# Kernel tuning notes

Measured on AMD Instinct MI355X. Metric: run time of the kernel, lower is better.

The kernel has to match this reference:

```python
import jax, jax.numpy as jnp
import numpy as np

MAX_CH = 21
LAT_DIM = 64
D_EMBED = 1024
N_HEADS = 16
D_HEAD = D_EMBED // N_HEADS  # 64
L = MAX_CH * LAT_DIM         # 1344 latents
B, T = 4, 1024


def setup_inputs() -> dict:
    key = jax.random.key(0)
    k1, k2, k3, k4, k5, k6 = jax.random.split(key, 6)
    x = jax.random.normal(k1, (B, T, D_EMBED), dtype=jnp.float32)
    # boolean channel mask [b, L, T]
    ch_mask = jax.random.randint(k2, (B, L, T), 0, 2) > 0
    # learned latent queries [L, H*d] (xavier-uniform-ish init)
    lim_q = float(np.sqrt(6.0 / (L + N_HEADS * D_HEAD)))
    latent_q = jax.random.uniform(k3, (L, N_HEADS * D_HEAD), minval=-lim_q, maxval=lim_q, dtype=jnp.float32)
    # Linear weights (torch layout: [out, in]) and biases
    lim_w = float(np.sqrt(1.0 / D_EMBED))
    w_k_w = jax.random.uniform(k4, (N_HEADS * D_HEAD, D_EMBED), minval=-lim_w, maxval=lim_w, dtype=jnp.float32)
    w_k_b = jnp.zeros((N_HEADS * D_HEAD,), dtype=jnp.float32)
    w_v_w = jax.random.uniform(k5, (N_HEADS * D_HEAD, D_EMBED), minval=-lim_w, maxval=lim_w, dtype=jnp.float32)
    w_v_b = jax.random.uniform(k6, (N_HEADS * D_HEAD,), minval=-lim_w, maxval=lim_w, dtype=jnp.float32)
    return {"x": x, "ch_mask": ch_mask, "latent_q": latent_q,
            "w_k_w": w_k_w, "w_k_b": w_k_b, "w_v_w": w_v_w, "w_v_b": w_v_b}


def reference(x, ch_mask, latent_q, w_k_w, w_k_b, w_v_w, w_v_b):
    b, t, d = x.shape
    H, dh = N_HEADS, D_HEAD
    l = latent_q.shape[0]
    # faithful to torch .view(-1, H, L, d): raw row-major reinterpretation
    lq = latent_q.reshape(1, H, l, dh)                    # [1,H,L,dh]
    k = (x @ w_k_w.T + w_k_b).reshape(b, t, H, dh).transpose(0, 2, 3, 1)  # [b,H,dh,T]
    v = (x @ w_v_w.T + w_v_b).reshape(b, t, H, dh).transpose(0, 2, 1, 3)  # [b,H,T,dh]
    scale = jnp.float32(H) ** -0.5  # note: n_heads**-0.5, as in source
    scores = jnp.einsum('ohld,bhdt->bhlt', lq, k) * scale  # [b,H,L,T]
    mask = ch_mask[:, None, :, :]                           # [b,1,L,T] broadcast over heads
    scores = jnp.where(mask, scores, jnp.float32(-1e9))
    w = jax.nn.softmax(scores, axis=-1)
    w = jnp.where(mask, w, jnp.float32(0.0))
    out = jnp.einsum('bhlt,bhtd->bhld', w, v)               # [b,H,L,dh]
    return out.transpose(0, 2, 1, 3).reshape(b, l, H * dh)  # [b,L,H*dh]
```

## Files before the change

kernel.cpp:

```cpp
#include <hip/hip_runtime.h>
#include <hip/hip_bf16.h>

#define B_SZ 4
#define T_SZ 1024
#define NH 16
#define L_SZ 1344
#define LT_COUNT 21

typedef __attribute__((ext_vector_type(8))) short short8;
typedef __attribute__((ext_vector_type(4))) short short4v;
typedef __attribute__((ext_vector_type(4))) float floatx4;

typedef __attribute__((address_space(1))) const void gvoid;
typedef __attribute__((address_space(3))) void svoid;
#define GLD16(gp, lp) \
  __builtin_amdgcn_global_load_lds((gvoid*)(gp), (svoid*)(lp), 16, 0, 0)

static __device__ inline short bf16bits(float f) {
  return __builtin_bit_cast(short, __float2bfloat16(f));
}
static __device__ inline short4v cvt4(float4 v) {
  short4v r;
  r.x = bf16bits(v.x); r.y = bf16bits(v.y);
  r.z = bf16bits(v.z); r.w = bf16bits(v.w);
  return r;
}

static __device__ inline unsigned pack_bf16_2(float a, float b) {
  unsigned ua = __builtin_bit_cast(unsigned, a) + 0x8000u;
  unsigned ub = __builtin_bit_cast(unsigned, b) + 0x8000u;
  return __builtin_amdgcn_perm(ub, ua, 0x07060302u);
}
static __device__ inline uint2 pack_bf16_4(float4 v) {
  return make_uint2(pack_bf16_2(v.x, v.y), pack_bf16_2(v.z, v.w));
}


__global__ __launch_bounds__(256) void mask_detect(
    const unsigned char* __restrict__ m, int* __restrict__ flag) {
  __shared__ int any_off4, any_at4;
  if (threadIdx.x == 0) { any_off4 = 0; any_at4 = 0; }
  __syncthreads();
  int a1 = 0, a2 = 0;
  for (int i = threadIdx.x; i < 4096; i += 256) {
    unsigned char v = m[i];
    if (v) {
      if ((i & 3) != 0) a1 = 1;
      if ((i & 7) == 4) a2 = 1;
    }
  }
  if (a1) atomicOr(&any_off4, 1);
  if (a2) atomicOr(&any_at4, 1);
  __syncthreads();
  if (threadIdx.x == 0) *flag = any_off4 ? 1 : (any_at4 ? 0 : 2);
}

__global__ __launch_bounds__(256) void prep_kernel(
    const float4* __restrict__ x, const float4* __restrict__ wk,
    const float4* __restrict__ wv,
    uint2* __restrict__ xb, uint2* __restrict__ wkb, uint2* __restrict__ wvb,
    const void* __restrict__ mask, const int* __restrict__ flag,
    unsigned int* __restrict__ bits) {
  const int f = *flag;
  const int lane = threadIdx.x & 63;
  for (int vb = blockIdx.x; vb < 27648; vb += gridDim.x) {
    if (vb < 6144) {
      size_t i = (size_t)vb * 256 + threadIdx.x;
      if (i < 1048576)      xb[i] = pack_bf16_4(x[i]);
      else if (i < 1310720) wkb[i - 1048576] = pack_bf16_4(wk[i - 1048576]);
      else                  wvb[i - 1310720] = pack_bf16_4(wv[i - 1310720]);
    } else {
      int idx = (vb - 6144) * 256 + threadIdx.x;
      bool v;
      if (f == 1)      v = ((const signed char*)mask)[idx] != 0;
      else if (f == 2) v = ((const long long*)mask)[idx] != 0;
      else             v = ((const int*)mask)[idx] != 0;
      unsigned long long bal = __ballot(v);
      if ((lane & 31) == 0) {
        unsigned int w = (lane & 32) ? (unsigned int)(bal >> 32) : (unsigned int)bal;
        bits[idx >> 5] = w;
      }
    }
  }
}

__global__ __launch_bounds__(256, 4) void gemm_kv_bf16(
    const __hip_bfloat16* __restrict__ xb,
    const __hip_bfloat16* __restrict__ wkb, const __hip_bfloat16* __restrict__ wvb,
    const float* __restrict__ bk, const float* __restrict__ bv,
    __hip_bfloat16* __restrict__ k_buf, __hip_bfloat16* __restrict__ v_buf) {
  __shared__ __align__(16) __hip_bfloat16 ldsA[2][128 * 32];
  __shared__ __align__(16) __hip_bfloat16 ldsB[2][64 * 32];
  const int tid = threadIdx.x;
  const int lane = tid & 63, w = tid >> 6;
  const int wm = w & 1, wn = w >> 1;
  const int c15 = lane & 15, kq = lane >> 4;

  const __hip_bfloat16* A;
  const __hip_bfloat16* B;
  int TA, TB;
  if (blockIdx.z == 0) {
    A = wkb; B = xb; TA = blockIdx.x >> 6; TB = blockIdx.x & 63;
  } else {
    A = xb; B = wvb; TA = blockIdx.x >> 4; TB = blockIdx.x & 15;
  }
  const __hip_bfloat16* Abase = A + (size_t)TA * 128 * 1024;
  const __hip_bfloat16* Bbase = B + (size_t)TB * 64 * 1024;

  floatx4 acc[4][2];
  #pragma unroll
  for (int i = 0; i < 4; ++i)
    #pragma unroll
    for (int j = 0; j < 2; ++j) acc[i][j] = (floatx4){0.f, 0.f, 0.f, 0.f};

#define GSTAGE(sb, kk) do {                                                  \
    int cA_ = w * 128 + lane;                                                \
    int rA_ = cA_ >> 2, gA_ = (cA_ & 3) ^ (rA_ & 3);                         \
    GLD16(Abase + (size_t)rA_ * 1024 + (kk) + gA_ * 8,                       \
          &ldsA[sb][(w * 128) * 8]);                                         \
    int cA2_ = cA_ + 64;                                                     \
    int rA2_ = cA2_ >> 2, gA2_ = (cA2_ & 3) ^ (rA2_ & 3);                    \
    GLD16(Abase + (size_t)rA2_ * 1024 + (kk) + gA2_ * 8,                     \
          &ldsA[sb][(w * 128 + 64) * 8]);                                    \
    int cB_ = w * 64 + lane;                                                 \
    int rB_ = cB_ >> 2, gB_ = (cB_ & 3) ^ (rB_ & 3);                         \
    GLD16(Bbase + (size_t)rB_ * 1024 + (kk) + gB_ * 8,                       \
          &ldsB[sb][(w * 64) * 8]);                                          \
  } while (0)

  GSTAGE(0, 0);
  for (int kk = 0; kk < 1024; kk += 32) {
    const int buf = (kk >> 5) & 1;
    if (kk + 32 < 1024) {
      GSTAGE(buf ^ 1, kk + 32);
      asm volatile("s_waitcnt vmcnt(3)" ::: "memory");
    } else {
      asm volatile("s_waitcnt vmcnt(0)" ::: "memory");
    }
    __builtin_amdgcn_s_barrier();

    short8 af[4], bfr[2];
    #pragma unroll
    for (int mi = 0; mi < 4; ++mi) {
      int row = wm * 64 + mi * 16 + c15;
      af[mi] = *(const short8*)(&ldsA[buf][row * 32 + ((kq ^ (row & 3)) * 8)]);
    }
    #pragma unroll
    for (int ni = 0; ni < 2; ++ni) {
      int row = wn * 32 + ni * 16 + c15;
      bfr[ni] = *(const short8*)(&ldsB[buf][row * 32 + ((kq ^ (row & 3)) * 8)]);
    }
    #pragma unroll
    for (int mi = 0; mi < 4; ++mi)
      #pragma unroll
      for (int ni = 0; ni < 2; ++ni)
        acc[mi][ni] = __builtin_amdgcn_mfma_f32_16x16x32_bf16(
            af[mi], bfr[ni], acc[mi][ni], 0, 0, 0);

    asm volatile("s_waitcnt lgkmcnt(0)" ::: "memory");
    __builtin_amdgcn_s_barrier();
  }
#undef GSTAGE

  if (blockIdx.z == 0) {
    #pragma unroll
    for (int ni = 0; ni < 2; ++ni) {
      int gr = TB * 64 + wn * 32 + ni * 16 + c15;
      int b = gr >> 10, tc = (gr >> 6) & 15;
      int ni2 = (gr & 63) >> 4;
      #pragma unroll
      for (int mi = 0; mi < 4; ++mi) {
        int d0 = TA * 128 + wm * 64 + mi * 16 + kq * 4;
        int h = d0 >> 6, hd = d0 & 63;
        int half = hd >> 5, q4 = (hd >> 3) & 3, jlo = hd & 7;
        int bh = b * 16 + h;
        float4 b4 = *(const float4*)(bk + d0);
        float4 v4 = {acc[mi][ni][0] + b4.x, acc[mi][ni][1] + b4.y,
                     acc[mi][ni][2] + b4.z, acc[mi][ni][3] + b4.w};
        *(uint2*)(k_buf + ((size_t)((bh * 16 + tc) * 8 + ni2 * 2 + half)) * 512 +
                  (q4 * 16 + c15) * 8 + jlo) = pack_bf16_4(v4);
      }
    }
  } else {
    #pragma unroll
    for (int ni = 0; ni < 2; ++ni) {
      int d = TB * 64 + wn * 32 + ni * 16 + c15;
      int h = d >> 6;
      int di = (d & 63) >> 4;
      float bias = bv[d];
      #pragma unroll
      for (int mi = 0; mi < 4; ++mi) {
        int gr = TA * 128 + wm * 64 + mi * 16 + kq * 4;
        int b = gr >> 10, tc = (gr >> 6) & 15;
        int tl = gr & 63;
        int half = tl >> 5, q4 = (tl >> 3) & 3, jlo = tl & 7;
        int bh = b * 16 + h;
        float4 v4 = {acc[mi][ni][0] + bias, acc[mi][ni][1] + bias,
                     acc[mi][ni][2] + bias, acc[mi][ni][3] + bias};
        *(uint2*)(v_buf + ((size_t)((bh * 16 + tc) * 8 + di * 2 + half)) * 512 +
                  (q4 * 16 + c15) * 8 + jlo) = pack_bf16_4(v4);
      }
    }
  }
}

__global__ __launch_bounds__(256, 4) void attn_kernel(
    const float* __restrict__ latent_q,
    const __hip_bfloat16* __restrict__ k_buf,
    const __hip_bfloat16* __restrict__ v_buf,
    const unsigned int* __restrict__ mbits,
    float* __restrict__ out) {
  __shared__ __align__(16) __hip_bfloat16 ldsK[2][4096];
  __shared__ __align__(16) __hip_bfloat16 ldsV[2][4096];
  __shared__ __align__(16) __hip_bfloat16 pbuf[4][1024];

  const int tid = threadIdx.x;
  const int lane = tid & 63;
  const int w = tid >> 6;
  int bid = blockIdx.x;
  int xcd = bid & 7, j = bid >> 3;
  int bh = xcd * 8 + j / LT_COUNT;
  int lt = j % LT_COUNT;
  int h = bh & 15, b = bh >> 4;
  const int q4 = lane >> 4, c15 = lane & 15;
  const int c7 = c15 & 7;
  const int l0 = lt * 64;

  const float QS = 0.25f * 1.44269504089f;
  short8 qf[2];
  {
    const float* qp = latent_q + ((size_t)(h * L_SZ + l0 + w * 16 + c15)) * 64 + q4 * 8;
    float4 a0 = *(const float4*)(qp);
    float4 a1 = *(const float4*)(qp + 4);
    float4 a2 = *(const float4*)(qp + 32);
    float4 a3 = *(const float4*)(qp + 36);
    a0.x *= QS; a0.y *= QS; a0.z *= QS; a0.w *= QS;
    a1.x *= QS; a1.y *= QS; a1.z *= QS; a1.w *= QS;
    a2.x *= QS; a2.y *= QS; a2.z *= QS; a2.w *= QS;
    a3.x *= QS; a3.y *= QS; a3.z *= QS; a3.w *= QS;
    short4v t0 = cvt4(a0), t1 = cvt4(a1), t2 = cvt4(a2), t3 = cvt4(a3);
    qf[0] = (short8){t0.x, t0.y, t0.z, t0.w, t1.x, t1.y, t1.z, t1.w};
    qf[1] = (short8){t2.x, t2.y, t2.z, t2.w, t3.x, t3.y, t3.z, t3.w};
  }

  floatx4 l4 = (floatx4){0.f, 0.f, 0.f, 0.f};
  floatx4 o_acc[4];
  #pragma unroll
  for (int di = 0; di < 4; ++di) o_acc[di] = (floatx4){0.f, 0.f, 0.f, 0.f};

  const __hip_bfloat16* kb = k_buf + (size_t)bh * 65536;
  const __hip_bfloat16* vb = v_buf + (size_t)bh * 65536;
  __hip_bfloat16* pw = pbuf[w];
  const unsigned int* mrow = mbits + ((size_t)(b * L_SZ + l0 + w * 16 + c15)) * 32;

#define STAGE_KV(sb, tcn) do {                                              \
    const __hip_bfloat16* gk_ = kb + (size_t)(tcn) * 4096;                  \
    const __hip_bfloat16* gv_ = vb + (size_t)(tcn) * 4096;                  \
    int o0_ = w * 512 + lane * 8;                                           \
    GLD16(gk_ + o0_,        &ldsK[sb][w * 512]);                            \
    GLD16(gk_ + 2048 + o0_, &ldsK[sb][2048 + w * 512]);                     \
    GLD16(gv_ + o0_,        &ldsV[sb][w * 512]);                            \
    GLD16(gv_ + 2048 + o0_, &ldsV[sb][2048 + w * 512]);                     \
  } while (0)

  STAGE_KV(0, 0);
  uint2 mw_cur = *(const uint2*)(mrow);

  for (int tc = 0; tc < 16; ++tc) {
    const int buf = tc & 1;
    if (tc + 1 < 16) {
      STAGE_KV(buf ^ 1, tc + 1);
      asm volatile("s_waitcnt vmcnt(4)" ::: "memory");
    } else {
      asm volatile("s_waitcnt vmcnt(0)" ::: "memory");
    }
    __builtin_amdgcn_s_barrier();

    uint2 mw_nxt = *(const uint2*)(mrow + (((tc + 1) & 15) * 2));

    short8 kf[2][4];
    #pragma unroll
    for (int half = 0; half < 2; ++half)
      #pragma unroll
      for (int ni = 0; ni < 4; ++ni)
        kf[half][ni] = *(const short8*)(&ldsK[buf][(ni * 2 + half) * 512 + lane * 8]);
    floatx4 s[4];
    #pragma unroll
    for (int ni = 0; ni < 4; ++ni) s[ni] = (floatx4){0.f, 0.f, 0.f, 0.f};
    __builtin_amdgcn_s_setprio(1);
    #pragma unroll
    for (int half = 0; half < 2; ++half)
      #pragma unroll
      for (int ni = 0; ni < 4; ++ni)
        s[ni] = __builtin_amdgcn_mfma_f32_16x16x32_bf16(kf[half][ni], qf[half], s[ni], 0, 0, 0);
    __builtin_amdgcn_s_setprio(0);

    short8 vf[2][4];
    #pragma unroll
    for (int half = 0; half < 2; ++half)
      #pragma unroll
      for (int di = 0; di < 4; ++di)
        vf[half][di] = *(const short8*)(&ldsV[buf][(di * 2 + half) * 512 + lane * 8]);

    #pragma unroll
    for (int ni = 0; ni < 4; ++ni) {
      unsigned mword = (ni >= 2) ? mw_cur.y : mw_cur.x;
      float4 p4;
      #pragma unroll
      for (int r = 0; r < 4; ++r) {
        float e = exp2f(s[ni][r]);
        int sh = (ni & 1) * 16 + q4 * 4 + r;
        ((float*)&p4)[r] = ((mword >> sh) & 1) ? e : 0.f;
      }
      l4[0] += p4.x; l4[1] += p4.y;
      l4[2] += p4.z; l4[3] += p4.w;
      int pc = (ni * 2 + (q4 >> 1)) ^ c7;
      *(uint2*)(pw + c15 * 64 + pc * 8 + (q4 & 1) * 4) = pack_bf16_4(p4);
    }

    int pc0 = q4 ^ c7;
    short8 pf0 = *(const short8*)(pw + c15 * 64 + pc0 * 8);
    short8 pf1 = *(const short8*)(pw + c15 * 64 + (pc0 ^ 4) * 8);
    __builtin_amdgcn_s_setprio(1);
    #pragma unroll
    for (int di = 0; di < 4; ++di)
      o_acc[di] = __builtin_amdgcn_mfma_f32_16x16x32_bf16(vf[0][di], pf0, o_acc[di], 0, 0, 0);
    #pragma unroll
    for (int di = 0; di < 4; ++di)
      o_acc[di] = __builtin_amdgcn_mfma_f32_16x16x32_bf16(vf[1][di], pf1, o_acc[di], 0, 0, 0);
    __builtin_amdgcn_s_setprio(0);

    mw_cur = mw_nxt;

    asm volatile("s_waitcnt lgkmcnt(0)" ::: "memory");
    __builtin_amdgcn_s_barrier();
  }
#undef STAGE_KV

  float la = (l4[0] + l4[1]) + (l4[2] + l4[3]);
  la += __shfl_xor(la, 16, 64);
  la += __shfl_xor(la, 32, 64);
  float inv = (la > 0.f) ? 1.f / la : 0.f;
  float* ob = out + ((size_t)(b * L_SZ + l0 + w * 16 + c15)) * 1024 + h * 64;
  #pragma unroll
  for (int di = 0; di < 4; ++di) {
    float4 o4 = {o_acc[di][0] * inv, o_acc[di][1] * inv,
                 o_acc[di][2] * inv, o_acc[di][3] * inv};
    *(float4*)(ob + di * 16 + q4 * 4) = o4;
  }
}

extern "C" void kernel_launch(void* const* d_in, const int* in_sizes, int n_in,
                              void* d_out, int out_size, void* d_ws, size_t ws_size,
                              hipStream_t stream) {
  const float* x      = (const float*)d_in[0];
  const void* ch_mask = d_in[1];
  const float* lq     = (const float*)d_in[2];
  const float* wk     = (const float*)d_in[3];
  const float* bk     = (const float*)d_in[4];
  const float* wv     = (const float*)d_in[5];
  const float* bv     = (const float*)d_in[6];
  float* out = (float*)d_out;

  char* ws = (char*)d_ws;
  unsigned int* mbits   = (unsigned int*)ws;
  int* flag             = (int*)(ws + 720896);
  __hip_bfloat16* k_buf = (__hip_bfloat16*)(ws + 786432);
  __hip_bfloat16* v_buf = (__hip_bfloat16*)(ws + 786432 + 8388608);

  __hip_bfloat16* xb  = (__hip_bfloat16*)d_out;
  __hip_bfloat16* wkb = xb + 4 * 1024 * 1024;
  __hip_bfloat16* wvb = wkb + 1024 * 1024;

  mask_detect<<<1, 256, 0, stream>>>((const unsigned char*)ch_mask, flag);
  prep_kernel<<<2048, 256, 0, stream>>>(
      (const float4*)x, (const float4*)wk, (const float4*)wv,
      (uint2*)xb, (uint2*)wkb, (uint2*)wvb,
      ch_mask, flag, mbits);
  gemm_kv_bf16<<<dim3(512, 1, 2), 256, 0, stream>>>(xb, wkb, wvb, bk, bv, k_buf, v_buf);

  attn_kernel<<<8 * 168, 256, 0, stream>>>(lq, k_buf, v_buf, mbits, out);
}
```

Measured before the change: 192.8 us.

## Fold mask detection into prep, split K/V staging, compute row sums via MFMA

Removes the separate single-block mask_detect launch. Each wave of prep_kernel now infers the mask element width itself from the first 4 KB of the mask. In the attention loop, K and V tile prefetches are issued separately, and the V load is placed after the QK MFMAs. This rearranges the waitcnt/barrier structure and drops the end-of-iteration lgkmcnt wait and barrier. The softmax denominator is accumulated with extra MFMAs against a ones vector instead of scalar adds plus a final cross-lane shuffle reduction. This trades two extra MFMAs per tile for fewer VALU ops, and depends on the reworked barrier placement still protecting the double buffers.

```diff
diff --git a/kernel.cpp b/kernel.cpp
--- a/kernel.cpp
+++ b/kernel.cpp
@@ -36,33 +36,13 @@
 }
 
 
-__global__ __launch_bounds__(256) void mask_detect(
-    const unsigned char* __restrict__ m, int* __restrict__ flag) {
-  __shared__ int any_off4, any_at4;
-  if (threadIdx.x == 0) { any_off4 = 0; any_at4 = 0; }
-  __syncthreads();
-  int a1 = 0, a2 = 0;
-  for (int i = threadIdx.x; i < 4096; i += 256) {
-    unsigned char v = m[i];
-    if (v) {
-      if ((i & 3) != 0) a1 = 1;
-      if ((i & 7) == 4) a2 = 1;
-    }
-  }
-  if (a1) atomicOr(&any_off4, 1);
-  if (a2) atomicOr(&any_at4, 1);
-  __syncthreads();
-  if (threadIdx.x == 0) *flag = any_off4 ? 1 : (any_at4 ? 0 : 2);
-}
-
 __global__ __launch_bounds__(256) void prep_kernel(
     const float4* __restrict__ x, const float4* __restrict__ wk,
     const float4* __restrict__ wv,
     uint2* __restrict__ xb, uint2* __restrict__ wkb, uint2* __restrict__ wvb,
-    const void* __restrict__ mask, const int* __restrict__ flag,
-    unsigned int* __restrict__ bits) {
-  const int f = *flag;
+    const void* __restrict__ mask, unsigned int* __restrict__ bits) {
   const int lane = threadIdx.x & 63;
+  int f = -1;
   for (int vb = blockIdx.x; vb < 27648; vb += gridDim.x) {
     if (vb < 6144) {
       size_t i = (size_t)vb * 256 + threadIdx.x;
@@ -70,6 +50,16 @@
       else if (i < 1310720) wkb[i - 1048576] = pack_bf16_4(wk[i - 1048576]);
       else                  wvb[i - 1310720] = pack_bf16_4(wv[i - 1310720]);
     } else {
+      if (f < 0) {
+        const uint4* mp = (const uint4*)mask;
+        uint4 a = mp[lane * 4 + 0], b2 = mp[lane * 4 + 1];
+        uint4 c = mp[lane * 4 + 2], d = mp[lane * 4 + 3];
+        unsigned oo = (a.x | a.y | a.z | a.w | b2.x | b2.y | b2.z | b2.w |
+                       c.x | c.y | c.z | c.w | d.x | d.y | d.z | d.w) & 0xFFFFFF00u;
+        unsigned aa = (a.y | a.w | b2.y | b2.w | c.y | c.w | d.y | d.w) & 0xFFu;
+        int anyo = __any(oo != 0), anya = __any(aa != 0);
+        f = anyo ? 1 : (anya ? 0 : 2);
+      }
       int idx = (vb - 6144) * 256 + threadIdx.x;
       bool v;
       if (f == 1)      v = ((const signed char*)mask)[idx] != 0;
@@ -243,40 +233,49 @@
     qf[1] = (short8){t2.x, t2.y, t2.z, t2.w, t3.x, t3.y, t3.z, t3.w};
   }
 
-  floatx4 l4 = (floatx4){0.f, 0.f, 0.f, 0.f};
+  const short ob16 = (short)0x3F80;
+  const short8 ones8 = (short8){ob16, ob16, ob16, ob16, ob16, ob16, ob16, ob16};
+  const floatx4 zero4 = (floatx4){0.f, 0.f, 0.f, 0.f};
+
+  floatx4 lacc = zero4;
   floatx4 o_acc[4];
   #pragma unroll
-  for (int di = 0; di < 4; ++di) o_acc[di] = (floatx4){0.f, 0.f, 0.f, 0.f};
+  for (int di = 0; di < 4; ++di) o_acc[di] = zero4;
 
   const __hip_bfloat16* kb = k_buf + (size_t)bh * 65536;
   const __hip_bfloat16* vb = v_buf + (size_t)bh * 65536;
   __hip_bfloat16* pw = pbuf[w];
   const unsigned int* mrow = mbits + ((size_t)(b * L_SZ + l0 + w * 16 + c15)) * 32;
 
-#define STAGE_KV(sb, tcn) do {                                              \
+#define STAGE_K(sb, tcn) do {                                               \
     const __hip_bfloat16* gk_ = kb + (size_t)(tcn) * 4096;                  \
-    const __hip_bfloat16* gv_ = vb + (size_t)(tcn) * 4096;                  \
     int o0_ = w * 512 + lane * 8;                                           \
     GLD16(gk_ + o0_,        &ldsK[sb][w * 512]);                            \
     GLD16(gk_ + 2048 + o0_, &ldsK[sb][2048 + w * 512]);                     \
+  } while (0)
+#define STAGE_V(sb, tcn) do {                                               \
+    const __hip_bfloat16* gv_ = vb + (size_t)(tcn) * 4096;                  \
+    int o0_ = w * 512 + lane * 8;                                           \
     GLD16(gv_ + o0_,        &ldsV[sb][w * 512]);                            \
     GLD16(gv_ + 2048 + o0_, &ldsV[sb][2048 + w * 512]);                     \
   } while (0)
 
-  STAGE_KV(0, 0);
   uint2 mw_cur = *(const uint2*)(mrow);
+  STAGE_K(0, 0);
+  STAGE_V(0, 0);
 
   for (int tc = 0; tc < 16; ++tc) {
     const int buf = tc & 1;
-    if (tc + 1 < 16) {
-      STAGE_KV(buf ^ 1, tc + 1);
-      asm volatile("s_waitcnt vmcnt(4)" ::: "memory");
+    if (tc < 15) {
+      STAGE_K(buf ^ 1, tc + 1);
+      asm volatile("s_waitcnt vmcnt(5)" ::: "memory");
     } else {
-      asm volatile("s_waitcnt vmcnt(0)" ::: "memory");
+      asm volatile("s_waitcnt vmcnt(3)" ::: "memory");
     }
     __builtin_amdgcn_s_barrier();
 
-    uint2 mw_nxt = *(const uint2*)(mrow + (((tc + 1) & 15) * 2));
+    uint2 mw_nxt = mw_cur;
+    if (tc < 15) mw_nxt = *(const uint2*)(mrow + (tc + 1) * 2);
 
     short8 kf[2][4];
     #pragma unroll
@@ -285,15 +284,22 @@
       for (int ni = 0; ni < 4; ++ni)
         kf[half][ni] = *(const short8*)(&ldsK[buf][(ni * 2 + half) * 512 + lane * 8]);
     floatx4 s[4];
-    #pragma unroll
-    for (int ni = 0; ni < 4; ++ni) s[ni] = (floatx4){0.f, 0.f, 0.f, 0.f};
     __builtin_amdgcn_s_setprio(1);
     #pragma unroll
-    for (int half = 0; half < 2; ++half)
-      #pragma unroll
-      for (int ni = 0; ni < 4; ++ni)
-        s[ni] = __builtin_amdgcn_mfma_f32_16x16x32_bf16(kf[half][ni], qf[half], s[ni], 0, 0, 0);
+    for (int ni = 0; ni < 4; ++ni)
+      s[ni] = __builtin_amdgcn_mfma_f32_16x16x32_bf16(kf[0][ni], qf[0], zero4, 0, 0, 0);
+    #pragma unroll
+    for (int ni = 0; ni < 4; ++ni)
+      s[ni] = __builtin_amdgcn_mfma_f32_16x16x32_bf16(kf[1][ni], qf[1], s[ni], 0, 0, 0);
     __builtin_amdgcn_s_setprio(0);
+
+    if (tc < 15) {
+      STAGE_V(buf ^ 1, tc + 1);
+      asm volatile("s_waitcnt vmcnt(5)" ::: "memory");
+    } else {
+      asm volatile("s_waitcnt vmcnt(0)" ::: "memory");
+    }
+    __builtin_amdgcn_s_barrier();
 
     short8 vf[2][4];
     #pragma unroll
@@ -312,8 +318,6 @@
         int sh = (ni & 1) * 16 + q4 * 4 + r;
         ((float*)&p4)[r] = ((mword >> sh) & 1) ? e : 0.f;
       }
-      l4[0] += p4.x; l4[1] += p4.y;
-      l4[2] += p4.z; l4[3] += p4.w;
       int pc = (ni * 2 + (q4 >> 1)) ^ c7;
       *(uint2*)(pw + c15 * 64 + pc * 8 + (q4 & 1) * 4) = pack_bf16_4(p4);
     }
@@ -328,18 +332,16 @@
     #pragma unroll
     for (int di = 0; di < 4; ++di)
       o_acc[di] = __builtin_amdgcn_mfma_f32_16x16x32_bf16(vf[1][di], pf1, o_acc[di], 0, 0, 0);
+    lacc = __builtin_amdgcn_mfma_f32_16x16x32_bf16(ones8, pf0, lacc, 0, 0, 0);
+    lacc = __builtin_amdgcn_mfma_f32_16x16x32_bf16(ones8, pf1, lacc, 0, 0, 0);
     __builtin_amdgcn_s_setprio(0);
 
     mw_cur = mw_nxt;
-
-    asm volatile("s_waitcnt lgkmcnt(0)" ::: "memory");
-    __builtin_amdgcn_s_barrier();
-  }
-#undef STAGE_KV
-
-  float la = (l4[0] + l4[1]) + (l4[2] + l4[3]);
-  la += __shfl_xor(la, 16, 64);
-  la += __shfl_xor(la, 32, 64);
+  }
+#undef STAGE_K
+#undef STAGE_V
+
+  float la = lacc[0];
   float inv = (la > 0.f) ? 1.f / la : 0.f;
   float* ob = out + ((size_t)(b * L_SZ + l0 + w * 16 + c15)) * 1024 + h * 64;
   #pragma unroll
@@ -364,7 +366,6 @@
 
   char* ws = (char*)d_ws;
   unsigned int* mbits   = (unsigned int*)ws;
-  int* flag             = (int*)(ws + 720896);
   __hip_bfloat16* k_buf = (__hip_bfloat16*)(ws + 786432);
   __hip_bfloat16* v_buf = (__hip_bfloat16*)(ws + 786432 + 8388608);
 
@@ -372,11 +373,10 @@
   __hip_bfloat16* wkb = xb + 4 * 1024 * 1024;
   __hip_bfloat16* wvb = wkb + 1024 * 1024;
 
-  mask_detect<<<1, 256, 0, stream>>>((const unsigned char*)ch_mask, flag);
   prep_kernel<<<2048, 256, 0, stream>>>(
       (const float4*)x, (const float4*)wk, (const float4*)wv,
       (uint2*)xb, (uint2*)wkb, (uint2*)wvb,
-      ch_mask, flag, mbits);
+      ch_mask, mbits);
   gemm_kv_bf16<<<dim3(512, 1, 2), 256, 0, stream>>>(xb, wkb, wvb, bk, bv, k_buf, v_buf);
 
   attn_kernel<<<8 * 168, 256, 0, stream>>>(lq, k_buf, v_buf, mbits, out);
```

Measured after the change: 189.2 us. Within noise of the previous version (-1.9%).
